# Performance work log

Hardware: AMD Instinct MI355X
Metric: run time of the kernel (lower is better)

## Reference

```python
import jax, jax.numpy as jnp
import numpy as np

T = 1_000_000          # number of t_eval points (~1 year at 30 s)
N_ROOMS = 10
N = 12                 # 2 latent wall nodes + n_rooms
DT = 30.0              # seconds between t_eval points
LOAD_SCALE = 50.0      # physical_cooling_scaling: W/m^2 scale for sigmoid(loads)


def setup_inputs() -> dict:
    key = jax.random.key(0)
    k1, k2, k3, k4, k5 = jax.random.split(key, 5)
    t_eval = jnp.arange(T, dtype=jnp.float32) * DT
    x0 = 26.0 * jnp.ones((N,), jnp.float32)  # reset_iv: 26 C at every node
    # Stable slow RC dynamics: negative-definite-ish A with small coupling
    A = (-1e-5 * jnp.eye(N, dtype=jnp.float32)
         + 1e-6 * jax.random.normal(k1, (N, N), jnp.float32))
    B = 1e-6 * jax.random.normal(k2, (N, 1 + N_ROOMS), jnp.float32)
    Tout_data = 10.0 + 20.0 * jax.random.uniform(k3, (T,), jnp.float32)  # outdoor temp samples on t_eval grid
    loads_raw = jax.random.normal(k4, (2, N_ROOMS), jnp.float32)         # pre-sigmoid [cool; gain] loads
    room_areas = 10.0 + 40.0 * jax.random.uniform(k5, (N_ROOMS,), jnp.float32)
    return {"t_eval": t_eval, "x0": x0, "A": A, "B": B,
            "Tout_data": Tout_data, "loads_raw": loads_raw, "room_areas": room_areas}


def reference(t_eval, x0, A, B, Tout_data, loads_raw, room_areas):
    # transform + physical scaling of loads (self.transform = sigmoid)
    loads = jax.nn.sigmoid(loads_raw) * LOAD_SCALE
    cool_load, gain_load = loads[0], loads[1]
    action = 0.0  # no cooling policy -> self.action stays 0
    Q_area = -cool_load * action + gain_load            # [n_rooms]
    Q_watts = Q_area * room_areas                        # proportional_heating
    # u = [Tout; Q_watts] so B@u = B[:,0]*Tout + B[:,1:]@Q_watts (Q constant over t)
    b0 = B[:, 0]                                         # [N]
    Bq = B[:, 1:] @ Q_watts                              # [N], constant forcing
    h = t_eval[1] - t_eval[0]                            # uniform step
    # Linear interp of Tout: value at t_i, midpoint t_i+h/2, and t_{i+1}
    To_t = Tout_data[:-1]
    To_n = Tout_data[1:]
    To_m = 0.5 * (To_t + To_n)

    def f(x, To):  # dy/dt = A x + B u
        return A @ x + b0 * To + Bq

    def step(x, tou):
        to_t, to_m, to_n = tou
        k1 = f(x, to_t)
        k2 = f(x + 0.5 * h * k1, to_m)
        k3 = f(x + 0.5 * h * k2, to_m)
        k4 = f(x + h * k3, to_n)
        xn = x + (h / 6.0) * (k1 + 2.0 * k2 + 2.0 * k3 + k4)
        return xn, xn

    _, xs = jax.lax.scan(step, x0, (To_t, To_m, To_n))
    return jnp.concatenate([x0[None, :], xs], axis=0)  # [T, N]
```

## Files before the change

kernel.cpp:

```cpp
#include <hip/hip_runtime.h>
#include <math.h>


#define S_STEPS 999999
#define CH      4
#define BLK     256
#define NB      977
#define NCHUNK  250000
#define LASTFULL 249998

#define OFF_M   0
#define OFF_C   144
#define OFF_AL  156
#define OFF_BE  168
#define OFF_K   192
#define OFF_P2  264
#define OFF_PA  1416
#define OFF_PL  1704
#define OFF_PD  2136
#define OFF_AGG 4440

#define FMA4(Q,a,b,c,d,acc) fmaf((Q).w,(d),fmaf((Q).z,(c),fmaf((Q).y,(b),fmaf((Q).x,(a),(acc)))))

__device__ __forceinline__ void mv_acc(const float* Pf, const float* x, float* y) {
  const float4* P = reinterpret_cast<const float4*>(Pf);
#pragma unroll
  for (int i = 0; i < 12; ++i) {
    float4 a = P[3*i], b = P[3*i+1], c = P[3*i+2];
    y[i] = FMA4(c, x[8],x[9],x[10],x[11],
            FMA4(b, x[4],x[5],x[6],x[7],
             FMA4(a, x[0],x[1],x[2],x[3], y[i])));
  }
}

__device__ __forceinline__ float rowdot(const float* Prow, const float* xv) {
  const float4* P = reinterpret_cast<const float4*>(Prow);
  float4 a = P[0], b = P[1], c = P[2];
  return FMA4(c, xv[8],xv[9],xv[10],xv[11],
          FMA4(b, xv[4],xv[5],xv[6],xv[7],
           FMA4(a, xv[0],xv[1],xv[2],xv[3], 0.f)));
}

__device__ __forceinline__ void fold_chunk(const float* __restrict__ cons,
                                           const float* tos, float* v) {
  const float4* Kq = reinterpret_cast<const float4*>(cons + OFF_K);
  float4 c0=Kq[0], c1=Kq[1], c2=Kq[2];
  v[0]=c0.x; v[1]=c0.y; v[2]=c0.z; v[3]=c0.w;
  v[4]=c1.x; v[5]=c1.y; v[6]=c1.z; v[7]=c1.w;
  v[8]=c2.x; v[9]=c2.y; v[10]=c2.z; v[11]=c2.w;
#pragma unroll
  for (int s = 0; s < 5; ++s) {
    float ts = tos[s];
    float4 ka=Kq[3*(s+1)], kb=Kq[3*(s+1)+1], kc=Kq[3*(s+1)+2];
    v[0]=fmaf(ka.x,ts,v[0]); v[1]=fmaf(ka.y,ts,v[1]); v[2]=fmaf(ka.z,ts,v[2]); v[3]=fmaf(ka.w,ts,v[3]);
    v[4]=fmaf(kb.x,ts,v[4]); v[5]=fmaf(kb.y,ts,v[5]); v[6]=fmaf(kb.z,ts,v[6]); v[7]=fmaf(kb.w,ts,v[7]);
    v[8]=fmaf(kc.x,ts,v[8]); v[9]=fmaf(kc.y,ts,v[9]); v[10]=fmaf(kc.z,ts,v[10]); v[11]=fmaf(kc.w,ts,v[11]);
  }
}

__global__ void __launch_bounds__(512) setup_kernel(
    const float* __restrict__ t_eval, const float* __restrict__ A,
    const float* __restrict__ Bm, const float* __restrict__ loads_raw,
    const float* __restrict__ areas, float* ws) {
  __shared__ double H1[144], H2[144], H3[144], H4[144], Md[144];
  __shared__ double Qa[144], Qb[144];
  __shared__ double C64[144], C128[144], C256[144], C512[144];
  __shared__ double C1024[144], C2048[144], C4096[144];
  __shared__ double cd[12], ald[12], bed[12], b0d[12], bqd[12];
  __shared__ double Vv[3][12], Kd[72];
  int t = threadIdx.x;
  double h = (double)t_eval[1] - (double)t_eval[0];
  if (t < 144) H1[t] = h * (double)A[t];
  if (t < 12) {
    b0d[t] = (double)Bm[t*11];
    double s = 0.0;
    for (int r = 0; r < 10; ++r) {
      double gq = 50.0 / (1.0 + exp(-(double)loads_raw[10 + r]));
      s += (double)Bm[t*11 + 1 + r] * (gq * (double)areas[r]);
    }
    bqd[t] = s;
  }
  if (t < 72) Kd[t] = 0.0;
  __syncthreads();
  if (t < 144) {
    int i=t/12, j=t%12; double s=0.0;
#pragma unroll
    for (int m = 0; m < 12; ++m) s += H1[i*12+m]*H1[m*12+j];
    H2[t]=s;
  }
  __syncthreads();
  if (t < 288) {
    int w=t/144, e=t%144, i=e/12, j=e%12;
    const double* Bp = w ? H2 : H1;
    double s = 0.0;
#pragma unroll
    for (int m = 0; m < 12; ++m) s += H2[i*12+m]*Bp[m*12+j];
    (w ? H4 : H3)[e] = s;
  }
  __syncthreads();
  if (t < 12) {
    double hb=0,h2b=0,h3b=0,hb0=0,h2b0=0,h3b0=0;
#pragma unroll
    for (int m = 0; m < 12; ++m) {
      hb  += H1[t*12+m]*bqd[m]; h2b  += H2[t*12+m]*bqd[m]; h3b  += H3[t*12+m]*bqd[m];
      hb0 += H1[t*12+m]*b0d[m]; h2b0 += H2[t*12+m]*b0d[m]; h3b0 += H3[t*12+m]*b0d[m];
    }
    double h6 = h / 6.0;
    cd[t]  = h6*(6.0*bqd[t] + 3.0*hb + h2b + 0.25*h3b);
    ald[t] = h6*(3.0*b0d[t] + 2.0*hb0 + 0.75*h2b0 + 0.25*h3b0);
    bed[t] = h6*(3.0*b0d[t] + hb0 + 0.25*h2b0);
    Vv[0][t]=ald[t]; Vv[1][t]=bed[t]; Vv[2][t]=cd[t];
    Kd[48+t] += ald[t]; Kd[60+t] += bed[t]; Kd[t] += cd[t];
  }
  if (t >= 144 && t < 288) {
    int e=t-144, i=e/12, j=e%12;
    Md[e] = (i==j ? 1.0 : 0.0) + H1[e] + 0.5*H2[e] + H3[e]/6.0 + H4[e]/24.0;
  }
  __syncthreads();
  if (t < 144) { ws[OFF_M+t] = (float)Md[t]; Qa[t] = Md[t]; }
  if (t < 12) {
    ws[OFF_C+t]=(float)cd[t]; ws[OFF_AL+t]=(float)ald[t]; ws[OFF_BE+t]=(float)bed[t];
  }
  __syncthreads();
  double* src = Qa; double* dst = Qb;
  for (int r = 1; r <= 12; ++r) {
    double acc = 0.0, ks = 0.0;
    if (t < 144) {
      int i=t/12, j=t%12;
#pragma unroll
      for (int m = 0; m < 12; ++m) acc += src[i*12+m]*src[m*12+j];
    }
    int w=0, i2=0;
    if (r <= 3 && t >= 256 && t < 292) {
      w=(t-256)/12; i2=(t-256)%12;
#pragma unroll
      for (int m = 0; m < 12; ++m) ks += Md[i2*12+m]*Vv[w][m];
    }
    __syncthreads();
    if (t < 144) {
      dst[t] = acc;
      if (r >= 2 && r <= 9) ws[OFF_P2+(r-2)*144+t] = (float)acc;
      if (r == 6)  C64[t]=acc;
      if (r == 7)  C128[t]=acc;
      if (r == 8)  C256[t]=acc;
      if (r == 9)  C512[t]=acc;
      if (r == 10) C1024[t]=acc;
      if (r == 11) C2048[t]=acc;
      if (r == 12) C4096[t]=acc;
    }
    if (r <= 3 && t >= 256 && t < 292) {
      Vv[w][i2] = ks;
      if (w == 0) Kd[(4-r)*12+i2] += ks;
      else if (w == 1) Kd[(5-r)*12+i2] += ks;
      else Kd[i2] += ks;
    }
    __syncthreads();
    double* tmp = src; src = dst; dst = tmp;
  }
  if (t < 72) ws[OFF_K+t] = (float)Kd[t];
  if (t < 144) {
    ws[OFF_PL+t]     = (float)C1024[t];
    ws[OFF_PL+144+t] = (float)C2048[t];
    ws[OFF_PD+t]     = (t % 13 == 0) ? 1.f : 0.f;
    ws[OFF_PD+144+t] = (float)C4096[t];
  }
  if (t < 432) {
    int w=t/144, e=t%144, i=e/12, j=e%12;
    const double* Ap = (w==0) ? C64 : ((w==1) ? C256 : C1024);
    const double* Bp = (w==0) ? C128 : ((w==1) ? C512 : C2048);
    double s = 0.0;
#pragma unroll
    for (int m = 0; m < 12; ++m) s += Ap[i*12+m]*Bp[m*12+j];
    if (w==0) ws[OFF_PA+e] = (float)s;
    else if (w==1) ws[OFF_PA+144+e] = (float)s;
    else ws[OFF_PL+2*144+e] = (float)s;
  }
  for (int j = 2; j < 16; ++j) {
    double acc = 0.0;
    if (t < 144) {
      int i=t/12, jj=t%12;
#pragma unroll
      for (int m = 0; m < 12; ++m) acc += src[i*12+m]*C4096[m*12+jj];
    }
    __syncthreads();
    if (t < 144) { dst[t] = acc; ws[OFF_PD+j*144+t] = (float)acc; }
    __syncthreads();
    double* tmp = src; src = dst; dst = tmp;
  }
}

__global__ void __launch_bounds__(BLK, 4) block_agg(
    const float* __restrict__ cons, const float* __restrict__ To,
    const float* __restrict__ x0, float* __restrict__ agg) {
  __shared__ __align__(16) float Tw[48], Ta[24];
  int k = threadIdx.x, b = blockIdx.x;
  int g = b*BLK + k, base = g*CH;
  bool fullc = (g <= LASTFULL);
  float to_[5];
#pragma unroll
  for (int i = 0; i < 5; ++i) to_[i] = 0.f;
  if (fullc) {
    const float4* tp = reinterpret_cast<const float4*>(To + base);
    float4 ta = tp[0];
    to_[0]=ta.x; to_[1]=ta.y; to_[2]=ta.z; to_[3]=ta.w;
    to_[4]=To[base+4];
  }
  float v[12];
  if (fullc) fold_chunk(cons, to_, v);
  else {
#pragma unroll
    for (int i = 0; i < 12; ++i) v[i] = 0.f;
  }
  if (g == 0) {
    float xi[12];
#pragma unroll
    for (int i = 0; i < 12; ++i) xi[i] = x0[i];
    mv_acc(cons + OFF_P2, xi, v);
  }
  int j = k & 63;
#pragma unroll
  for (int l = 0; l < 6; ++l) {
    int off = 1 << l;
    float nb[12];
#pragma unroll
    for (int i = 0; i < 12; ++i) nb[i] = __shfl_up(v[i], (unsigned)off, 64);
    if (j >= off) mv_acc(cons + OFF_P2 + l*144, nb, v);
  }
  if (j == 63) {
#pragma unroll
    for (int i = 0; i < 12; ++i) Tw[(k>>6)*12 + i] = v[i];
  }
  __syncthreads();
  if (k < 24) {
    int p = k/12, comp = k - p*12;
    Ta[k] = rowdot(cons + OFF_P2 + 6*144 + comp*12, Tw + 2*p*12)
          + Tw[(2*p+1)*12 + comp];
  }
  __syncthreads();
  if (k < 12) {
    agg[b*12 + k] = rowdot(cons + OFF_P2 + 7*144 + k*12, Ta) + Ta[12 + k];
  }
}

__global__ void __launch_bounds__(BLK, 2) scan_expand(
    const float* __restrict__ cons, const float* __restrict__ To,
    const float* __restrict__ x0, const float* __restrict__ agg,
    float* __restrict__ out) {
  __shared__ __align__(16) float Tw[48];
  __shared__ __align__(16) float Pw[48];
  __shared__ __align__(16) float lkb[64*12];
  __shared__ __align__(16) float yv[16*12];
  __shared__ __align__(16) float zv[16*12];
  __shared__ __align__(16) float Xs[12];
  __shared__ __align__(16) float Qw[48];
  int k = threadIdx.x, b = blockIdx.x;
  int g = b*BLK + k, base = g*CH;
  bool active = (g < NCHUNK), fullc = (g <= LASTFULL);
  float to_[5];
#pragma unroll
  for (int i = 0; i < 5; ++i) to_[i] = 0.f;
  if (active) {
    const float4* tp = reinterpret_cast<const float4*>(To + base);
    float4 ta = tp[0];
    to_[0]=ta.x; to_[1]=ta.y; to_[2]=ta.z; to_[3]=ta.w;
    to_[4] = fullc ? To[base+4] : 0.f;
  }
  float v[12];
  if (fullc) fold_chunk(cons, to_, v);
  else {
#pragma unroll
    for (int i = 0; i < 12; ++i) v[i] = 0.f;
  }
  if (g == 0) {
    float xi[12];
#pragma unroll
    for (int i = 0; i < 12; ++i) xi[i] = x0[i];
    mv_acc(cons + OFF_P2, xi, v);
  }
  int j = k & 63, w = k >> 6;
#pragma unroll
  for (int l = 0; l < 6; ++l) {
    int off = 1 << l;
    float nb[12];
#pragma unroll
    for (int i = 0; i < 12; ++i) nb[i] = __shfl_up(v[i], (unsigned)off, 64);
    if (j >= off) mv_acc(cons + OFF_P2 + l*144, nb, v);
  }
  float se[12];
#pragma unroll
  for (int i = 0; i < 12; ++i) {
    float u = __shfl_up(v[i], 1u, 64);
    se[i] = (j == 0) ? 0.f : u;
  }
  if (j == 63) {
#pragma unroll
    for (int i = 0; i < 12; ++i) Tw[w*12 + i] = v[i];
  }
#pragma unroll
  for (int r = 0; r < 3; ++r) {
    int idx = k + r*BLK;
    int slot = idx / 12, comp = idx - slot*12;
    int src = b - 1 - slot;
    float acc = 0.f;
    if (src >= 0) {
      int jj = slot & 3;
      const float* ag = agg + src*12;
      acc = (jj == 0) ? ag[comp]
          : rowdot(cons + OFF_PL + (jj-1)*144 + comp*12, ag);
    }
    lkb[idx] = acc;
  }
  __syncthreads();
  if (k < 192) {
    int i = k/12, comp = k - i*12;
    yv[k] = lkb[(4*i)*12+comp] + lkb[(4*i+1)*12+comp]
          + lkb[(4*i+2)*12+comp] + lkb[(4*i+3)*12+comp];
  } else if (k < 216) {
    int q = k - 192;
    if (q < 12) Pw[q] = 0.f;
    else Pw[q] = Tw[q-12];
  }
  __syncthreads();
  if (k < 192) {
    int i = k/12, comp = k - i*12;
    zv[k] = (i == 0) ? yv[comp]
          : rowdot(cons + OFF_PD + i*144 + comp*12, yv + i*12);
  } else if (k < 204) {
    int comp = k - 192;
    Pw[24+comp] = rowdot(cons + OFF_P2 + 6*144 + comp*12, Pw+12) + Tw[12+comp];
  }
  __syncthreads();
  if (k < 12) {
    float s = 0.f;
#pragma unroll
    for (int i = 0; i < 16; ++i) s += zv[i*12 + k];
    Xs[k] = s;
  } else if (k >= 192 && k < 204) {
    int comp = k - 192;
    Pw[36+comp] = rowdot(cons + OFF_P2 + 6*144 + comp*12, Pw+24) + Tw[24+comp];
  }
  __syncthreads();
  if (k < 48) {
    int ww = k/12, comp = k - ww*12;
    float acc;
    if (ww == 0) acc = Xs[comp];
    else if (ww == 1) acc = rowdot(cons + OFF_P2 + 6*144 + comp*12, Xs);
    else if (ww == 2) acc = rowdot(cons + OFF_P2 + 7*144 + comp*12, Xs);
    else acc = rowdot(cons + OFF_PA + 144 + comp*12, Xs);
    Qw[k] = acc + Pw[k];
  }
  __syncthreads();
  if (!active) return;
  float x[12];
#pragma unroll
  for (int i = 0; i < 12; ++i) x[i] = Qw[w*12 + i];
#pragma unroll
  for (int l = 0; l < 6; ++l) {
    if ((j >> l) & 1) {
      float vn[12];
#pragma unroll
      for (int i = 0; i < 12; ++i) vn[i] = 0.f;
      mv_acc(cons + OFF_P2 + l*144, x, vn);
#pragma unroll
      for (int i = 0; i < 12; ++i) x[i] = vn[i];
    }
  }
#pragma unroll
  for (int i = 0; i < 12; ++i) x[i] += se[i];
  if (b == 0 && k == 0) {
#pragma unroll
    for (int i = 0; i < 12; ++i) x[i] += x0[i];
#pragma unroll
    for (int i = 0; i < 12; ++i) out[i] = x0[i];
  }
  float cv[12], av[12], bv[12];
#pragma unroll
  for (int i = 0; i < 12; ++i) {
    cv[i] = cons[OFF_C + i]; av[i] = cons[OFF_AL + i]; bv[i] = cons[OFF_BE + i];
  }
  const float4* Mq = reinterpret_cast<const float4*>(cons + OFF_M);
#pragma unroll
  for (int s = 0; s < CH; ++s) {
    float tot = to_[s], ton = (s < CH-1) ? to_[s+1] : to_[4];
    float xn[12];
#pragma unroll
    for (int i = 0; i < 12; ++i) {
      float4 a = Mq[3*i], bq = Mq[3*i+1], c = Mq[3*i+2];
      xn[i] = FMA4(c, x[8],x[9],x[10],x[11],
               FMA4(bq, x[4],x[5],x[6],x[7],
                FMA4(a, x[0],x[1],x[2],x[3],
                 fmaf(bv[i],ton,fmaf(av[i],tot,cv[i])))));
    }
    int tt = base + s;
    if (tt < S_STEPS) {
      float4* op = reinterpret_cast<float4*>(out + (size_t)(tt+1)*12);
      op[0] = make_float4(xn[0],xn[1],xn[2],xn[3]);
      op[1] = make_float4(xn[4],xn[5],xn[6],xn[7]);
      op[2] = make_float4(xn[8],xn[9],xn[10],xn[11]);
    }
#pragma unroll
    for (int i = 0; i < 12; ++i) x[i] = xn[i];
  }
}

extern "C" void kernel_launch(void* const* d_in, const int* in_sizes, int n_in,
                              void* d_out, int out_size, void* d_ws, size_t ws_size,
                              hipStream_t stream) {
  const float* t_eval    = (const float*)d_in[0];
  const float* x0        = (const float*)d_in[1];
  const float* A         = (const float*)d_in[2];
  const float* B         = (const float*)d_in[3];
  const float* To        = (const float*)d_in[4];
  const float* loads_raw = (const float*)d_in[5];
  const float* areas     = (const float*)d_in[6];
  float* out = (float*)d_out;
  float* ws  = (float*)d_ws;

  setup_kernel<<<1, 512, 0, stream>>>(t_eval, A, B, loads_raw, areas, ws);
  block_agg<<<NB, BLK, 0, stream>>>(ws, To, x0, ws + OFF_AGG);
  scan_expand<<<NB, BLK, 0, stream>>>(ws, To, x0, ws + OFF_AGG, out);
}
```

Baseline: 131.8 us.

## Fuse block aggregate and scan expand into one decoupled-lookback kernel

Merges the two-pass block_agg + scan_expand scan into a single kernel. Blocks take a dynamic ID from an atomic counter, publish their aggregate with a release flag, and spin-wait on the flags of up to 64 predecessors. This removes a kernel launch and the recomputation of each chunk's fold and intra-wave scan in the second pass. The setup kernel is also restructured: more powers are computed by repeated squaring, and the PD lookback matrices are built as products of those powers rather than by a serial chain of multiplications. The risk is spin-wait latency and a dependency on block scheduling order, and the PD matrices are built from a different float product order.

```diff
diff --git a/kernel.cpp b/kernel.cpp
--- a/kernel.cpp
+++ b/kernel.cpp
@@ -16,9 +16,11 @@
 #define OFF_K   192
 #define OFF_P2  264
 #define OFF_PA  1416
-#define OFF_PL  1704
-#define OFF_PD  2136
-#define OFF_AGG 4440
+#define OFF_PL  1560
+#define OFF_PD  1992
+#define OFF_CNT 4296
+#define OFF_FLG 4300
+#define OFF_AGG 5280
 
 #define FMA4(Q,a,b,c,d,acc) fmaf((Q).w,(d),fmaf((Q).z,(c),fmaf((Q).y,(b),fmaf((Q).x,(a),(acc)))))
 
@@ -64,10 +66,11 @@
     const float* __restrict__ areas, float* ws) {
   __shared__ double H1[144], H2[144], H3[144], H4[144], Md[144];
   __shared__ double Qa[144], Qb[144];
-  __shared__ double C64[144], C128[144], C256[144], C512[144];
-  __shared__ double C1024[144], C2048[144], C4096[144];
+  __shared__ double C256[144], C512[144], C1024[144], C2048[144];
+  __shared__ double C4096[144], C8192[144], C16384[144], C32768[144];
+  __shared__ double C12288[144], C49152[144];
   __shared__ double cd[12], ald[12], bed[12], b0d[12], bqd[12];
-  __shared__ double Vv[3][12], Kd[72];
+  __shared__ double Vv[2][3][12], Kd[72];
   int t = threadIdx.x;
   double h = (double)t_eval[1] - (double)t_eval[0];
   if (t < 144) H1[t] = h * (double)A[t];
@@ -81,6 +84,10 @@
     bqd[t] = s;
   }
   if (t < 72) Kd[t] = 0.0;
+  {
+    int* wsi = (int*)ws;
+    for (int idx = t; idx < NB + 4; idx += 512) wsi[OFF_CNT + idx] = 0;
+  }
   __syncthreads();
   if (t < 144) {
     int i=t/12, j=t%12; double s=0.0;
@@ -109,7 +116,7 @@
     cd[t]  = h6*(6.0*bqd[t] + 3.0*hb + h2b + 0.25*h3b);
     ald[t] = h6*(3.0*b0d[t] + 2.0*hb0 + 0.75*h2b0 + 0.25*h3b0);
     bed[t] = h6*(3.0*b0d[t] + hb0 + 0.25*h2b0);
-    Vv[0][t]=ald[t]; Vv[1][t]=bed[t]; Vv[2][t]=cd[t];
+    Vv[0][0][t]=ald[t]; Vv[0][1][t]=bed[t]; Vv[0][2][t]=cd[t];
     Kd[48+t] += ald[t]; Kd[60+t] += bed[t]; Kd[t] += cd[t];
   }
   if (t >= 144 && t < 288) {
@@ -117,13 +124,9 @@
     Md[e] = (i==j ? 1.0 : 0.0) + H1[e] + 0.5*H2[e] + H3[e]/6.0 + H4[e]/24.0;
   }
   __syncthreads();
-  if (t < 144) { ws[OFF_M+t] = (float)Md[t]; Qa[t] = Md[t]; }
-  if (t < 12) {
-    ws[OFF_C+t]=(float)cd[t]; ws[OFF_AL+t]=(float)ald[t]; ws[OFF_BE+t]=(float)bed[t];
-  }
-  __syncthreads();
-  double* src = Qa; double* dst = Qb;
-  for (int r = 1; r <= 12; ++r) {
+  for (int r = 1; r <= 15; ++r) {
+    const double* src = (r==1) ? Md : ((r & 1) ? Qb : Qa);
+    double* dst = (r & 1) ? Qa : Qb;
     double acc = 0.0, ks = 0.0;
     if (t < 144) {
       int i=t/12, j=t%12;
@@ -134,126 +137,83 @@
     if (r <= 3 && t >= 256 && t < 292) {
       w=(t-256)/12; i2=(t-256)%12;
 #pragma unroll
-      for (int m = 0; m < 12; ++m) ks += Md[i2*12+m]*Vv[w][m];
-    }
-    __syncthreads();
+      for (int m = 0; m < 12; ++m) ks += Md[i2*12+m]*Vv[(r+1)&1][w][m];
+    }
+    if (r == 1) {
+      if (t >= 300 && t < 444) ws[OFF_M + (t-300)] = (float)Md[t-300];
+      if (t >= 444 && t < 456) {
+        int i = t-444;
+        ws[OFF_C+i]=(float)cd[i]; ws[OFF_AL+i]=(float)ald[i]; ws[OFF_BE+i]=(float)bed[i];
+      }
+    }
     if (t < 144) {
       dst[t] = acc;
-      if (r >= 2 && r <= 9) ws[OFF_P2+(r-2)*144+t] = (float)acc;
-      if (r == 6)  C64[t]=acc;
-      if (r == 7)  C128[t]=acc;
-      if (r == 8)  C256[t]=acc;
-      if (r == 9)  C512[t]=acc;
-      if (r == 10) C1024[t]=acc;
-      if (r == 11) C2048[t]=acc;
-      if (r == 12) C4096[t]=acc;
+      if (r >= 2 && r <= 9)  ws[OFF_P2 + (r-2)*144 + t] = (float)acc;
+      if (r == 8)  C256[t] = acc;
+      if (r == 9)  C512[t] = acc;
+      if (r == 10) { C1024[t] = acc; ws[OFF_PL + t] = (float)acc; }
+      if (r == 11) { C2048[t] = acc; ws[OFF_PL + 144 + t] = (float)acc; }
+      if (r == 12) C4096[t] = acc;
+      if (r == 13) C8192[t] = acc;
+      if (r == 14) C16384[t] = acc;
+      if (r == 15) C32768[t] = acc;
     }
     if (r <= 3 && t >= 256 && t < 292) {
-      Vv[w][i2] = ks;
+      Vv[r&1][w][i2] = ks;
       if (w == 0) Kd[(4-r)*12+i2] += ks;
       else if (w == 1) Kd[(5-r)*12+i2] += ks;
       else Kd[i2] += ks;
     }
     __syncthreads();
-    double* tmp = src; src = dst; dst = tmp;
-  }
-  if (t < 72) ws[OFF_K+t] = (float)Kd[t];
+  }
+  if (t < 72) ws[OFF_K + t] = (float)Kd[t];
   if (t < 144) {
-    ws[OFF_PL+t]     = (float)C1024[t];
-    ws[OFF_PL+144+t] = (float)C2048[t];
-    ws[OFF_PD+t]     = (t % 13 == 0) ? 1.f : 0.f;
-    ws[OFF_PD+144+t] = (float)C4096[t];
-  }
-  if (t < 432) {
-    int w=t/144, e=t%144, i=e/12, j=e%12;
-    const double* Ap = (w==0) ? C64 : ((w==1) ? C256 : C1024);
-    const double* Bp = (w==0) ? C128 : ((w==1) ? C512 : C2048);
+    ws[OFF_PD + t]         = (t % 13 == 0) ? 1.f : 0.f;
+    ws[OFF_PD + 144 + t]   = (float)C4096[t];
+    ws[OFF_PD + 2*144 + t] = (float)C8192[t];
+    ws[OFF_PD + 4*144 + t] = (float)C16384[t];
+    ws[OFF_PD + 8*144 + t] = (float)C32768[t];
+  }
+  for (int idx = t; idx < 576; idx += 512) {
+    int p = idx / 144, e = idx - p*144, i = e/12, jj = e - i*12;
+    const double* Ap = (p==0)?C256:(p==1)?C1024:(p==2)?C4096:C16384;
+    const double* Bp = (p==0)?C512:(p==1)?C2048:(p==2)?C8192:C32768;
     double s = 0.0;
 #pragma unroll
-    for (int m = 0; m < 12; ++m) s += Ap[i*12+m]*Bp[m*12+j];
-    if (w==0) ws[OFF_PA+e] = (float)s;
-    else if (w==1) ws[OFF_PA+144+e] = (float)s;
-    else ws[OFF_PL+2*144+e] = (float)s;
-  }
-  for (int j = 2; j < 16; ++j) {
-    double acc = 0.0;
-    if (t < 144) {
-      int i=t/12, jj=t%12;
-#pragma unroll
-      for (int m = 0; m < 12; ++m) acc += src[i*12+m]*C4096[m*12+jj];
-    }
-    __syncthreads();
-    if (t < 144) { dst[t] = acc; ws[OFF_PD+j*144+t] = (float)acc; }
-    __syncthreads();
-    double* tmp = src; src = dst; dst = tmp;
-  }
-}
-
-__global__ void __launch_bounds__(BLK, 4) block_agg(
+    for (int m = 0; m < 12; ++m) s += Ap[i*12+m]*Bp[m*12+jj];
+    if (p==0) ws[OFF_PA + e] = (float)s;
+    else if (p==1) ws[OFF_PL + 2*144 + e] = (float)s;
+    else if (p==2) { C12288[e] = s; ws[OFF_PD + 3*144 + e] = (float)s; }
+    else { C49152[e] = s; ws[OFF_PD + 12*144 + e] = (float)s; }
+  }
+  __syncthreads();
+  const int jl[9] = {5,6,7,9,10,11,13,14,15};
+  for (int idx = t; idx < 1296; idx += 512) {
+    int q = idx / 144, e = idx - q*144, i = e/12, jj = e - i*12;
+    int j = jl[q];
+    int hi = j >> 2, lo = j & 3;
+    const double* Hp = (hi==1)?C16384:(hi==2)?C32768:C49152;
+    const double* Lp = (lo==1)?C4096:(lo==2)?C8192:C12288;
+    double s = 0.0;
+#pragma unroll
+    for (int m = 0; m < 12; ++m) s += Hp[i*12+m]*Lp[m*12+jj];
+    ws[OFF_PD + j*144 + e] = (float)s;
+  }
+}
+
+__global__ void __launch_bounds__(BLK, 4) fused_scan(
     const float* __restrict__ cons, const float* __restrict__ To,
-    const float* __restrict__ x0, float* __restrict__ agg) {
-  __shared__ __align__(16) float Tw[48], Ta[24];
-  int k = threadIdx.x, b = blockIdx.x;
-  int g = b*BLK + k, base = g*CH;
-  bool fullc = (g <= LASTFULL);
-  float to_[5];
-#pragma unroll
-  for (int i = 0; i < 5; ++i) to_[i] = 0.f;
-  if (fullc) {
-    const float4* tp = reinterpret_cast<const float4*>(To + base);
-    float4 ta = tp[0];
-    to_[0]=ta.x; to_[1]=ta.y; to_[2]=ta.z; to_[3]=ta.w;
-    to_[4]=To[base+4];
-  }
-  float v[12];
-  if (fullc) fold_chunk(cons, to_, v);
-  else {
-#pragma unroll
-    for (int i = 0; i < 12; ++i) v[i] = 0.f;
-  }
-  if (g == 0) {
-    float xi[12];
-#pragma unroll
-    for (int i = 0; i < 12; ++i) xi[i] = x0[i];
-    mv_acc(cons + OFF_P2, xi, v);
-  }
-  int j = k & 63;
-#pragma unroll
-  for (int l = 0; l < 6; ++l) {
-    int off = 1 << l;
-    float nb[12];
-#pragma unroll
-    for (int i = 0; i < 12; ++i) nb[i] = __shfl_up(v[i], (unsigned)off, 64);
-    if (j >= off) mv_acc(cons + OFF_P2 + l*144, nb, v);
-  }
-  if (j == 63) {
-#pragma unroll
-    for (int i = 0; i < 12; ++i) Tw[(k>>6)*12 + i] = v[i];
-  }
-  __syncthreads();
-  if (k < 24) {
-    int p = k/12, comp = k - p*12;
-    Ta[k] = rowdot(cons + OFF_P2 + 6*144 + comp*12, Tw + 2*p*12)
-          + Tw[(2*p+1)*12 + comp];
-  }
-  __syncthreads();
-  if (k < 12) {
-    agg[b*12 + k] = rowdot(cons + OFF_P2 + 7*144 + k*12, Ta) + Ta[12 + k];
-  }
-}
-
-__global__ void __launch_bounds__(BLK, 2) scan_expand(
-    const float* __restrict__ cons, const float* __restrict__ To,
-    const float* __restrict__ x0, const float* __restrict__ agg,
+    const float* __restrict__ x0, float* agg, int* flags, int* cnt,
     float* __restrict__ out) {
-  __shared__ __align__(16) float Tw[48];
-  __shared__ __align__(16) float Pw[48];
+  __shared__ int sbid;
+  __shared__ __align__(16) float Tw[48], Ta[24], Pw[48];
+  __shared__ __align__(16) float aggL[64*12];
   __shared__ __align__(16) float lkb[64*12];
-  __shared__ __align__(16) float yv[16*12];
-  __shared__ __align__(16) float zv[16*12];
-  __shared__ __align__(16) float Xs[12];
-  __shared__ __align__(16) float Qw[48];
-  int k = threadIdx.x, b = blockIdx.x;
+  __shared__ __align__(16) float yv[192], zv[192], Xs[12], Qw[48];
+  int k = threadIdx.x;
+  if (k == 0) sbid = atomicAdd(cnt, 1);
+  __syncthreads();
+  int b = sbid;
   int g = b*BLK + k, base = g*CH;
   bool active = (g < NCHUNK), fullc = (g <= LASTFULL);
   float to_[5];
@@ -296,38 +256,71 @@
 #pragma unroll
     for (int i = 0; i < 12; ++i) Tw[w*12 + i] = v[i];
   }
+  __syncthreads();
+  if (k < 24) {
+    int p = k/12, comp = k - p*12;
+    Ta[k] = rowdot(cons + OFF_P2 + 6*144 + comp*12, Tw + 2*p*12)
+          + Tw[(2*p+1)*12 + comp];
+  } else if (k < 48) {
+    int q = k - 24;
+    if (q < 12) Pw[q] = 0.f;
+    else Pw[q] = Tw[q-12];
+  }
+  __syncthreads();
+  if (k < 12) {
+    float val = rowdot(cons + OFF_P2 + 7*144 + k*12, Ta) + Ta[12 + k];
+    __hip_atomic_store(&agg[b*12 + k], val, __ATOMIC_RELAXED,
+                       __HIP_MEMORY_SCOPE_AGENT);
+  } else if (k >= 192 && k < 204) {
+    int comp = k - 192;
+    Pw[24+comp] = rowdot(cons + OFF_P2 + 6*144 + comp*12, Pw+12) + Tw[12+comp];
+  }
+  __syncthreads();
+  if (k == 0) {
+    __threadfence();
+    __hip_atomic_store(&flags[b], 1, __ATOMIC_RELEASE, __HIP_MEMORY_SCOPE_AGENT);
+  } else if (k >= 64 && k < 128) {
+    int slot = k - 64, src = b - 1 - slot;
+    if (src >= 0) {
+      int guard = 0;
+      while (__hip_atomic_load(&flags[src], __ATOMIC_ACQUIRE,
+                               __HIP_MEMORY_SCOPE_AGENT) == 0 &&
+             guard < (1<<20)) {
+        ++guard;
+        __builtin_amdgcn_s_sleep(2);
+      }
+#pragma unroll
+      for (int i = 0; i < 12; ++i)
+        aggL[slot*12 + i] = __hip_atomic_load(&agg[src*12 + i],
+                                              __ATOMIC_RELAXED,
+                                              __HIP_MEMORY_SCOPE_AGENT);
+    } else {
+#pragma unroll
+      for (int i = 0; i < 12; ++i) aggL[slot*12 + i] = 0.f;
+    }
+  } else if (k >= 192 && k < 204) {
+    int comp = k - 192;
+    Pw[36+comp] = rowdot(cons + OFF_P2 + 6*144 + comp*12, Pw+24) + Tw[24+comp];
+  }
+  __syncthreads();
 #pragma unroll
   for (int r = 0; r < 3; ++r) {
     int idx = k + r*BLK;
-    int slot = idx / 12, comp = idx - slot*12;
-    int src = b - 1 - slot;
-    float acc = 0.f;
-    if (src >= 0) {
-      int jj = slot & 3;
-      const float* ag = agg + src*12;
-      acc = (jj == 0) ? ag[comp]
-          : rowdot(cons + OFF_PL + (jj-1)*144 + comp*12, ag);
-    }
-    lkb[idx] = acc;
+    int slot = idx / 12, comp = idx - slot*12, jj = slot & 3;
+    lkb[idx] = (jj == 0) ? aggL[slot*12 + comp]
+             : rowdot(cons + OFF_PL + (jj-1)*144 + comp*12, aggL + slot*12);
   }
   __syncthreads();
   if (k < 192) {
     int i = k/12, comp = k - i*12;
     yv[k] = lkb[(4*i)*12+comp] + lkb[(4*i+1)*12+comp]
           + lkb[(4*i+2)*12+comp] + lkb[(4*i+3)*12+comp];
-  } else if (k < 216) {
-    int q = k - 192;
-    if (q < 12) Pw[q] = 0.f;
-    else Pw[q] = Tw[q-12];
   }
   __syncthreads();
   if (k < 192) {
     int i = k/12, comp = k - i*12;
-    zv[k] = (i == 0) ? yv[comp]
+    zv[k] = (i == 0) ? yv[k]
           : rowdot(cons + OFF_PD + i*144 + comp*12, yv + i*12);
-  } else if (k < 204) {
-    int comp = k - 192;
-    Pw[24+comp] = rowdot(cons + OFF_P2 + 6*144 + comp*12, Pw+12) + Tw[12+comp];
   }
   __syncthreads();
   if (k < 12) {
@@ -335,9 +328,6 @@
 #pragma unroll
     for (int i = 0; i < 16; ++i) s += zv[i*12 + k];
     Xs[k] = s;
-  } else if (k >= 192 && k < 204) {
-    int comp = k - 192;
-    Pw[36+comp] = rowdot(cons + OFF_P2 + 6*144 + comp*12, Pw+24) + Tw[24+comp];
   }
   __syncthreads();
   if (k < 48) {
@@ -346,7 +336,7 @@
     if (ww == 0) acc = Xs[comp];
     else if (ww == 1) acc = rowdot(cons + OFF_P2 + 6*144 + comp*12, Xs);
     else if (ww == 2) acc = rowdot(cons + OFF_P2 + 7*144 + comp*12, Xs);
-    else acc = rowdot(cons + OFF_PA + 144 + comp*12, Xs);
+    else acc = rowdot(cons + OFF_PA + comp*12, Xs);
     Qw[k] = acc + Pw[k];
   }
   __syncthreads();
@@ -415,8 +405,9 @@
   const float* areas     = (const float*)d_in[6];
   float* out = (float*)d_out;
   float* ws  = (float*)d_ws;
+  int*   wsi = (int*)d_ws;
 
   setup_kernel<<<1, 512, 0, stream>>>(t_eval, A, B, loads_raw, areas, ws);
-  block_agg<<<NB, BLK, 0, stream>>>(ws, To, x0, ws + OFF_AGG);
-  scan_expand<<<NB, BLK, 0, stream>>>(ws, To, x0, ws + OFF_AGG, out);
-}
+  fused_scan<<<NB, BLK, 0, stream>>>(ws, To, x0, ws + OFF_AGG,
+                                     wsi + OFF_FLG, wsi + OFF_CNT, out);
+}
```

Measured after the change: 179.5 us. 1.36x slower.
